# Performance work log

Hardware: AMD Instinct MI355X
Metric: run time of the kernel (lower is better)

The kernel has to match this reference:

```python
import jax, jax.numpy as jnp
import numpy as np

N_NODES = 50000


def gcn_conv(x, edge_index, W, b, n_nodes):
    # Linear transform first (as in PyG GCNConv), then normalized aggregation
    xw = x @ W  # [N, out]
    src, dst = edge_index[0], edge_index[1]
    loops = jnp.arange(n_nodes, dtype=src.dtype)
    s = jnp.concatenate([src, loops])  # add self-loops
    d = jnp.concatenate([dst, loops])
    deg = jax.ops.segment_sum(jnp.ones_like(s, dtype=xw.dtype), d, num_segments=n_nodes)
    dinv = jnp.where(deg > 0, jax.lax.rsqrt(deg), 0.0)
    norm = dinv[s] * dinv[d]  # [E+N]
    msg = xw[s] * norm[:, None]  # gather + scale
    out = jax.ops.segment_sum(msg, d, num_segments=n_nodes)  # scatter-add
    return out + b


def setup_inputs() -> dict:
    key = jax.random.key(0)
    k1, k2, k3, k4 = jax.random.split(key, 4)
    in_dim, hidden = 128, 128
    n_edges = 625000
    x = jax.random.normal(k1, (N_NODES, in_dim), dtype=jnp.float32)
    edge_index = jax.random.randint(k2, (2, n_edges), 0, N_NODES, dtype=jnp.int64)
    # glorot-ish scale
    W1 = jax.random.normal(k3, (in_dim, hidden), dtype=jnp.float32) * (1.0 / np.sqrt(in_dim))
    b1 = jnp.zeros((hidden,), dtype=jnp.float32)
    W2 = jax.random.normal(k4, (hidden, hidden), dtype=jnp.float32) * (1.0 / np.sqrt(hidden))
    b2 = jnp.zeros((hidden,), dtype=jnp.float32)
    return {"x": x, "edge_index": edge_index, "W1": W1, "b1": b1, "W2": W2, "b2": b2}


def reference(x, edge_index, W1, b1, W2, b2):
    n = x.shape[0]
    h = gcn_conv(x, edge_index, W1, b1, n)
    h = jax.nn.relu(h)
    # dropout(p=0.3) is identity in eval mode
    h = gcn_conv(h, edge_index, W2, b2, n)
    return jax.nn.relu(h)
```

## Files before the change

### kernel.cpp

```cpp
#include <hip/hip_runtime.h>
#include <hip/hip_bf16.h>

#define NNODES 50000
#define BKT 64
#define LP 136
#define NC 25
#define CCAP 40960
#define P0EPT 16
#define FINE 256
#define AGG_BLOCKS 2048

typedef short bf16x8 __attribute__((ext_vector_type(8)));
typedef float f32x4 __attribute__((ext_vector_type(4)));

__device__ __forceinline__ unsigned short f2bf_rn(float f) {
    unsigned int u = __float_as_uint(f);
    return (unsigned short)((u + 0x7fffu + ((u >> 16) & 1u)) >> 16);
}
__device__ __forceinline__ float bf_lo(unsigned int u) { return __uint_as_float(u << 16); }
__device__ __forceinline__ float bf_hi(unsigned int u) { return __uint_as_float(u & 0xffff0000u); }


__global__ __launch_bounds__(256) void k_prep(const float* __restrict__ W1,
                                              const float* __restrict__ W2,
                                              unsigned short* __restrict__ WT1,
                                              unsigned short* __restrict__ WT2,
                                              const int* __restrict__ src,
                                              const int* __restrict__ dst,
                                              int* __restrict__ gcnt,
                                              unsigned int* __restrict__ rec, int E) {
    __shared__ float tile[128 * 129];
    int b = blockIdx.x, t = threadIdx.x;
    if (b < 2) {
        const float* W = b ? W2 : W1;
        unsigned short* WT = b ? WT2 : WT1;
        for (int idx = t; idx < 128 * 128; idx += 256)
            tile[(idx >> 7) * 129 + (idx & 127)] = W[idx];
        __syncthreads();
        for (int idx = t; idx < 128 * 128; idx += 256) {
            int c = idx >> 7, k = idx & 127;
            WT[c * 128 + k] = f2bf_rn(tile[k * 129 + c]);
        }
        return;
    }
    int* lhist = (int*)tile;
    int* lbase = lhist + NC;
    if (t < NC) lhist[t] = 0;
    __syncthreads();

    int e0 = ((b - 2) * 256 + t) * P0EPT;
    unsigned int r[P0EPT];
    int cc[P0EPT];
    int lofs[P0EPT];
    int nv = 0;
    if (e0 + P0EPT <= E) {
#pragma unroll
        for (int k4 = 0; k4 < P0EPT / 4; ++k4) {
            int4 s4 = *(const int4*)&src[e0 + k4 * 4];
            int4 d4 = *(const int4*)&dst[e0 + k4 * 4];
            int ss[4] = {s4.x, s4.y, s4.z, s4.w};
            int dd[4] = {d4.x, d4.y, d4.z, d4.w};
#pragma unroll
            for (int k = 0; k < 4; ++k) {
                r[k4 * 4 + k] = (unsigned)(ss[k] & 0xffff) | ((unsigned)dd[k] << 16);
                cc[k4 * 4 + k] = dd[k] >> 11;
            }
        }
        nv = P0EPT;
    } else {
#pragma unroll
        for (int k = 0; k < P0EPT; ++k) {
            int e = e0 + k;
            if (e < E) {
                int s = src[e], d = dst[e];
                r[k] = (unsigned)(s & 0xffff) | ((unsigned)d << 16);
                cc[k] = d >> 11;
                nv = k + 1;
            } else {
                cc[k] = 0;
            }
        }
    }
#pragma unroll
    for (int k = 0; k < P0EPT; ++k)
        if (k < nv) lofs[k] = atomicAdd(&lhist[cc[k]], 1);
    __syncthreads();
    if (t < NC) lbase[t] = atomicAdd(&gcnt[t], lhist[t]);
    __syncthreads();
#pragma unroll
    for (int k = 0; k < P0EPT; ++k)
        if (k < nv) {
            int pos = lbase[cc[k]] + lofs[k];
            if (pos < CCAP) rec[(size_t)cc[k] * CCAP + pos] = r[k];
        }
}


__global__ __launch_bounds__(256) void k_build(const unsigned int* __restrict__ rec,
                                               const int* __restrict__ gcnt,
                                               int* __restrict__ cnt,
                                               unsigned short* __restrict__ bkt,
                                               float* __restrict__ dinv,
                                               const float* __restrict__ X,
                                               const unsigned short* __restrict__ WT,
                                               unsigned short* __restrict__ Yb,
                                               int n, int P1B) {
    __shared__ __align__(16) unsigned char smem[FINE * BKT * 2 + FINE * 4];
    int t = threadIdx.x, b = blockIdx.x;
    if (b < P1B) {
        unsigned short* lbkt = (unsigned short*)smem;
        int* lcnt = (int*)(smem + FINE * BKT * 2);
        int lo = b * FINE;
        int c = lo >> 11;
        for (int i = t; i < FINE; i += 256) lcnt[i] = 0;
        __syncthreads();

        int M = min(gcnt[c], CCAP);
        const unsigned int* R = &rec[(size_t)c * CCAP];
        auto process = [&](unsigned int rv) {
            unsigned dl = (rv >> 16) - (unsigned)lo;
            if (dl < (unsigned)FINE) {
                int p = atomicAdd(&lcnt[dl], 1);
                if (p < BKT) lbkt[dl * BKT + p] = (unsigned short)(rv & 0xffffu);
            }
        };
        int M4 = M >> 2;
        for (int i = t; i < M4; i += 256) {
            uint4 q = *(const uint4*)&R[i * 4];
            process(q.x); process(q.y); process(q.z); process(q.w);
        }
        for (int i = (M4 << 2) + t; i < M; i += 256) process(R[i]);
        __syncthreads();

        if (lo + t < n) {
            int cv = lcnt[t];
            cnt[lo + t] = cv;
            dinv[lo + t] = rsqrtf((float)cv + 1.0f);
        }
        for (int i = t; i < FINE * 8; i += 256) {
            int node = i >> 3;
            if (lo + node < n)
                ((uint4*)&bkt[(size_t)lo * BKT])[i] = ((const uint4*)lbkt)[i];
        }
        return;
    }
    unsigned short* Ep = (unsigned short*)smem;
    int gb = b - P1B;
    int lane = t & 63, w = t >> 6;
    int m = lane & 15, quad = lane >> 4;
    int base = gb * 64 + w * 16;
    int row = min(base + m, n - 1);

    bf16x8 a[4];
#pragma unroll
    for (int kt = 0; kt < 4; ++kt) {
        const float* pa = &X[(size_t)row * 128 + kt * 32 + quad * 8];
        float4 v0 = *(const float4*)pa;
        float4 v1 = *(const float4*)(pa + 4);
        a[kt][0] = (short)f2bf_rn(v0.x); a[kt][1] = (short)f2bf_rn(v0.y);
        a[kt][2] = (short)f2bf_rn(v0.z); a[kt][3] = (short)f2bf_rn(v0.w);
        a[kt][4] = (short)f2bf_rn(v1.x); a[kt][5] = (short)f2bf_rn(v1.y);
        a[kt][6] = (short)f2bf_rn(v1.z); a[kt][7] = (short)f2bf_rn(v1.w);
    }

    f32x4 acc[8];
#pragma unroll
    for (int i = 0; i < 8; ++i) acc[i] = f32x4{0.f, 0.f, 0.f, 0.f};
#pragma unroll
    for (int kt = 0; kt < 4; ++kt) {
        int ko = kt * 32 + quad * 8;
#pragma unroll
        for (int ct = 0; ct < 8; ++ct) {
            bf16x8 bfrag = *(const bf16x8*)&WT[(ct * 16 + m) * 128 + ko];
            acc[ct] = __builtin_amdgcn_mfma_f32_16x16x32_bf16(a[kt], bfrag, acc[ct], 0, 0, 0);
        }
    }

    unsigned short* ep = &Ep[w * 16 * LP];
#pragma unroll
    for (int ct = 0; ct < 8; ++ct)
#pragma unroll
        for (int r = 0; r < 4; ++r)
            ep[(quad * 4 + r) * LP + ct * 16 + m] = f2bf_rn(acc[ct][r]);
    __syncthreads();
    int rr = lane & 15, cc2 = lane >> 4;
    int orow = base + rr;
    if (orow < n) {
#pragma unroll
        for (int i2 = 0; i2 < 4; ++i2)
            ((uint4*)&Yb[(size_t)orow * 128])[cc2 * 4 + i2] =
                *(const uint4*)&ep[rr * LP + (cc2 * 4 + i2) * 8];
    }
}


__device__ __forceinline__ void gather_wsum(const unsigned int* __restrict__ xwb,
                                            const float* __restrict__ dinv,
                                            const unsigned short* __restrict__ bp,
                                            int degc, int lane,
                                            float& ax, float& ay) {
    float px = 0.f, py = 0.f;
    int j = 0;
    for (; j + 8 <= degc; j += 8) {
        int4 q = *(const int4*)&bp[j];
        int s0 = q.x & 0xffff, s1 = (int)((unsigned)q.x >> 16);
        int s2 = q.y & 0xffff, s3 = (int)((unsigned)q.y >> 16);
        int s4 = q.z & 0xffff, s5 = (int)((unsigned)q.z >> 16);
        int s6 = q.w & 0xffff, s7 = (int)((unsigned)q.w >> 16);
        unsigned int u0 = xwb[(size_t)s0 * 64 + lane];
        unsigned int u1 = xwb[(size_t)s1 * 64 + lane];
        unsigned int u2 = xwb[(size_t)s2 * 64 + lane];
        unsigned int u3 = xwb[(size_t)s3 * 64 + lane];
        unsigned int u4 = xwb[(size_t)s4 * 64 + lane];
        unsigned int u5 = xwb[(size_t)s5 * 64 + lane];
        unsigned int u6 = xwb[(size_t)s6 * 64 + lane];
        unsigned int u7 = xwb[(size_t)s7 * 64 + lane];
        float w0 = dinv[s0], w1 = dinv[s1], w2 = dinv[s2], w3 = dinv[s3];
        float w4 = dinv[s4], w5 = dinv[s5], w6 = dinv[s6], w7 = dinv[s7];
        ax = fmaf(bf_lo(u0), w0, ax);  ay = fmaf(bf_hi(u0), w0, ay);
        px = fmaf(bf_lo(u1), w1, px);  py = fmaf(bf_hi(u1), w1, py);
        ax = fmaf(bf_lo(u2), w2, ax);  ay = fmaf(bf_hi(u2), w2, ay);
        px = fmaf(bf_lo(u3), w3, px);  py = fmaf(bf_hi(u3), w3, py);
        ax = fmaf(bf_lo(u4), w4, ax);  ay = fmaf(bf_hi(u4), w4, ay);
        px = fmaf(bf_lo(u5), w5, px);  py = fmaf(bf_hi(u5), w5, py);
        ax = fmaf(bf_lo(u6), w6, ax);  ay = fmaf(bf_hi(u6), w6, ay);
        px = fmaf(bf_lo(u7), w7, px);  py = fmaf(bf_hi(u7), w7, py);
    }
    if (j + 4 <= degc) {
        int2 q = *(const int2*)&bp[j];
        int s0 = q.x & 0xffff, s1 = (int)((unsigned)q.x >> 16);
        int s2 = q.y & 0xffff, s3 = (int)((unsigned)q.y >> 16);
        unsigned int u0 = xwb[(size_t)s0 * 64 + lane];
        unsigned int u1 = xwb[(size_t)s1 * 64 + lane];
        unsigned int u2 = xwb[(size_t)s2 * 64 + lane];
        unsigned int u3 = xwb[(size_t)s3 * 64 + lane];
        float w0 = dinv[s0], w1 = dinv[s1], w2 = dinv[s2], w3 = dinv[s3];
        ax = fmaf(bf_lo(u0), w0, ax);  ay = fmaf(bf_hi(u0), w0, ay);
        px = fmaf(bf_lo(u1), w1, px);  py = fmaf(bf_hi(u1), w1, py);
        ax = fmaf(bf_lo(u2), w2, ax);  ay = fmaf(bf_hi(u2), w2, ay);
        px = fmaf(bf_lo(u3), w3, px);  py = fmaf(bf_hi(u3), w3, py);
        j += 4;
    }
    for (; j < degc; ++j) {
        int s = bp[j];
        float wv = dinv[s];
        unsigned int u = xwb[(size_t)s * 64 + lane];
        ax = fmaf(bf_lo(u), wv, ax);
        ay = fmaf(bf_hi(u), wv, ay);
    }
    ax += px;
    ay += py;
}


__device__ __forceinline__ void gather_sum(const unsigned int* __restrict__ xwb,
                                           const unsigned short* __restrict__ bp,
                                           int degc, int lane,
                                           float& ax, float& ay) {
    float px = 0.f, py = 0.f;
    int j = 0;
    for (; j + 8 <= degc; j += 8) {
        int4 q = *(const int4*)&bp[j];
        int s0 = q.x & 0xffff, s1 = (int)((unsigned)q.x >> 16);
        int s2 = q.y & 0xffff, s3 = (int)((unsigned)q.y >> 16);
        int s4 = q.z & 0xffff, s5 = (int)((unsigned)q.z >> 16);
        int s6 = q.w & 0xffff, s7 = (int)((unsigned)q.w >> 16);
        unsigned int u0 = xwb[(size_t)s0 * 64 + lane];
        unsigned int u1 = xwb[(size_t)s1 * 64 + lane];
        unsigned int u2 = xwb[(size_t)s2 * 64 + lane];
        unsigned int u3 = xwb[(size_t)s3 * 64 + lane];
        unsigned int u4 = xwb[(size_t)s4 * 64 + lane];
        unsigned int u5 = xwb[(size_t)s5 * 64 + lane];
        unsigned int u6 = xwb[(size_t)s6 * 64 + lane];
        unsigned int u7 = xwb[(size_t)s7 * 64 + lane];
        ax += bf_lo(u0);  ay += bf_hi(u0);
        px += bf_lo(u1);  py += bf_hi(u1);
        ax += bf_lo(u2);  ay += bf_hi(u2);
        px += bf_lo(u3);  py += bf_hi(u3);
        ax += bf_lo(u4);  ay += bf_hi(u4);
        px += bf_lo(u5);  py += bf_hi(u5);
        ax += bf_lo(u6);  ay += bf_hi(u6);
        px += bf_lo(u7);  py += bf_hi(u7);
    }
    if (j + 4 <= degc) {
        int2 q = *(const int2*)&bp[j];
        int s0 = q.x & 0xffff, s1 = (int)((unsigned)q.x >> 16);
        int s2 = q.y & 0xffff, s3 = (int)((unsigned)q.y >> 16);
        unsigned int u0 = xwb[(size_t)s0 * 64 + lane];
        unsigned int u1 = xwb[(size_t)s1 * 64 + lane];
        unsigned int u2 = xwb[(size_t)s2 * 64 + lane];
        unsigned int u3 = xwb[(size_t)s3 * 64 + lane];
        ax += bf_lo(u0);  ay += bf_hi(u0);
        px += bf_lo(u1);  py += bf_hi(u1);
        ax += bf_lo(u2);  ay += bf_hi(u2);
        px += bf_lo(u3);  py += bf_hi(u3);
        j += 4;
    }
    for (; j < degc; ++j) {
        int s = bp[j];
        unsigned int u = xwb[(size_t)s * 64 + lane];
        ax += bf_lo(u);
        ay += bf_hi(u);
    }
    ax += px;
    ay += py;
}


__global__ __launch_bounds__(1024, 8) void k_aggemm(const unsigned int* __restrict__ xw1,
                                                    const int* __restrict__ cnt,
                                                    const unsigned short* __restrict__ bkt,
                                                    const float* __restrict__ dinv,
                                                    const float* __restrict__ bias,
                                                    const unsigned short* __restrict__ WT2,
                                                    unsigned short* __restrict__ xw2, int n) {
    __shared__ unsigned short Wl[128 * LP];
    __shared__ unsigned short At[64 * LP];
    __shared__ float dsw[64];
    int t = threadIdx.x, lane = t & 63, w = t >> 6;
    int m = lane & 15, quad = lane >> 4;
    int base = blockIdx.x * 64;

    for (int idx = t; idx < 128 * 16; idx += 1024) {
        int r = idx >> 4, c8 = (idx & 15) << 3;
        *(uint4*)&Wl[r * LP + c8] = *(const uint4*)&WT2[r * 128 + c8];
    }
    float bx = bias[lane * 2], by = bias[lane * 2 + 1];

#pragma unroll
    for (int k = 0; k < 4; ++k) {
        int nd = w * 4 + k;
        int i = min(base + nd, n - 1);
        int degc = min(cnt[i], BKT);
        float di = dinv[i];
        unsigned int v0 = xw1[(size_t)i * 64 + lane];
        float ax = di * bf_lo(v0), ay = di * bf_hi(v0);
        gather_wsum(xw1, dinv, &bkt[(size_t)i * BKT], degc, lane, ax, ay);
        ax = fmaxf(fmaf(di, ax, bx), 0.0f);
        ay = fmaxf(fmaf(di, ay, by), 0.0f);
        ((unsigned int*)&At[nd * LP])[lane] =
            (unsigned)f2bf_rn(ax) | ((unsigned)f2bf_rn(ay) << 16);
        if (lane == 0) dsw[nd] = di;
    }
    __syncthreads();

    int ct = w & 7, rb = w >> 3;
    f32x4 acc0 = f32x4{0.f, 0.f, 0.f, 0.f};
    f32x4 acc1 = f32x4{0.f, 0.f, 0.f, 0.f};
#pragma unroll
    for (int kt = 0; kt < 4; ++kt) {
        int ko = kt * 32 + quad * 8;
        bf16x8 bfrag = *(const bf16x8*)&Wl[(ct * 16 + m) * LP + ko];
        bf16x8 a0 = *(const bf16x8*)&At[(rb * 16 + m) * LP + ko];
        bf16x8 a1 = *(const bf16x8*)&At[((rb + 2) * 16 + m) * LP + ko];
        acc0 = __builtin_amdgcn_mfma_f32_16x16x32_bf16(a0, bfrag, acc0, 0, 0, 0);
        acc1 = __builtin_amdgcn_mfma_f32_16x16x32_bf16(a1, bfrag, acc1, 0, 0, 0);
    }
    __syncthreads();

#pragma unroll
    for (int r = 0; r < 4; ++r) {
        int r0 = rb * 16 + quad * 4 + r;
        int r1 = (rb + 2) * 16 + quad * 4 + r;
        At[r0 * LP + ct * 16 + m] = f2bf_rn(acc0[r] * dsw[r0]);
        At[r1 * LP + ct * 16 + m] = f2bf_rn(acc1[r] * dsw[r1]);
    }
    __syncthreads();

    int row = t >> 4, q = t & 15;
    int orow = base + row;
    if (orow < n)
        *(uint4*)&xw2[(size_t)orow * 128 + q * 8] = *(const uint4*)&At[row * LP + q * 8];
}


__global__ __launch_bounds__(256) void k_agg(const unsigned int* __restrict__ xwb,
                                             const int* __restrict__ cnt,
                                             const unsigned short* __restrict__ bkt,
                                             const float* __restrict__ dinv,
                                             const float* __restrict__ bias,
                                             float* __restrict__ out, int n) {
    int lane = threadIdx.x & 63;
    int gw = (blockIdx.x * 256 + threadIdx.x) >> 6;
    int nw = (gridDim.x * 256) >> 6;
    float bx = bias[lane * 2], by = bias[lane * 2 + 1];
    for (int i = gw; i < n; i += nw) {
        int degc = min(cnt[i], BKT);
        float di = dinv[i];
        unsigned int v0 = xwb[(size_t)i * 64 + lane];
        float ax = bf_lo(v0), ay = bf_hi(v0);
        gather_sum(xwb, &bkt[(size_t)i * BKT], degc, lane, ax, ay);
        ax = fmaxf(fmaf(di, ax, bx), 0.0f);
        ay = fmaxf(fmaf(di, ay, by), 0.0f);
        ((float2*)out)[(size_t)i * 64 + lane] = make_float2(ax, ay);
    }
}


extern "C" void kernel_launch(void* const* d_in, const int* in_sizes, int n_in,
                              void* d_out, int out_size, void* d_ws, size_t ws_size,
                              hipStream_t stream) {
    const float* x  = (const float*)d_in[0];
    const int*   ei = (const int*)d_in[1];
    const float* W1 = (const float*)d_in[2];
    const float* b1 = (const float*)d_in[3];
    const float* W2 = (const float*)d_in[4];
    const float* b2 = (const float*)d_in[5];
    float* out = (float*)d_out;

    const int N = NNODES;
    const int E = in_sizes[1] / 2;
    const int* src = ei;
    const int* dst = ei + E;

    char* p = (char*)d_ws;
    size_t off = 0;
    auto take = [&](size_t bytes) -> void* {
        void* r = p + off;
        off = (off + bytes + 255) & ~(size_t)255;
        return r;
    };
    int* cnt = (int*)take((size_t)N * 4);
    unsigned short* bkt = (unsigned short*)take((size_t)N * BKT * 2);
    unsigned short* w1t = (unsigned short*)take(128 * 128 * 2);
    unsigned short* w2t = (unsigned short*)take(128 * 128 * 2);
    unsigned short* xw1 = (unsigned short*)take((size_t)N * 128 * 2);
    unsigned short* xw2 = (unsigned short*)take((size_t)N * 128 * 2);
    float* dinv = (float*)take((size_t)N * 4);
    int* gcnt = (int*)take(NC * 4);
    unsigned int* rec = (unsigned int*)take((size_t)NC * CCAP * 4);

    const int P0B = (E + 256 * P0EPT - 1) / (256 * P0EPT);
    const int P1B = (N + FINE - 1) / FINE;
    const int GB = (N + 63) / 64;

    hipMemsetAsync(gcnt, 0, NC * sizeof(int), stream);
    k_prep<<<2 + P0B, 256, 0, stream>>>(W1, W2, w1t, w2t, src, dst, gcnt, rec, E);
    k_build<<<P1B + GB, 256, 0, stream>>>(rec, gcnt, cnt, bkt, dinv, x, w1t, xw1, N, P1B);
    k_aggemm<<<GB, 1024, 0, stream>>>((const unsigned int*)xw1, cnt, bkt, dinv,
                                      b1, w2t, xw2, N);
    k_agg<<<AGG_BLOCKS, 256, 0, stream>>>((const unsigned int*)xw2, cnt, bkt, dinv,
                                          b2, out, N);
}
```

Measured before the change: 179.7 us.

## Use finer coarse buckets and sentinel-padded bucket lists for half-wave gather

```diff
diff --git a/kernel.cpp b/kernel.cpp
--- a/kernel.cpp
+++ b/kernel.cpp
@@ -4,10 +4,11 @@
 #define NNODES 50000
 #define BKT 64
 #define LP 136
-#define NC 25
-#define CCAP 40960
+#define NC 196
+#define CCAP 4096
 #define P0EPT 16
 #define FINE 256
+#define SENT 50000
 #define AGG_BLOCKS 2048
 
 typedef short bf16x8 __attribute__((ext_vector_type(8)));
@@ -28,10 +29,20 @@
                                               const int* __restrict__ src,
                                               const int* __restrict__ dst,
                                               int* __restrict__ gcnt,
-                                              unsigned int* __restrict__ rec, int E) {
+                                              unsigned int* __restrict__ rec,
+                                              unsigned short* __restrict__ xw1,
+                                              unsigned short* __restrict__ xw2,
+                                              float* __restrict__ dinv, int E) {
     __shared__ float tile[128 * 129];
     int b = blockIdx.x, t = threadIdx.x;
     if (b < 2) {
+        if (b == 0) {
+            if (t < 64) {
+                ((unsigned int*)&xw1[(size_t)NNODES * 128])[t] = 0;
+                ((unsigned int*)&xw2[(size_t)NNODES * 128])[t] = 0;
+            }
+            if (t == 64) dinv[NNODES] = 0.0f;
+        }
         const float* W = b ? W2 : W1;
         unsigned short* WT = b ? WT2 : WT1;
         for (int idx = t; idx < 128 * 128; idx += 256)
@@ -63,7 +74,7 @@
 #pragma unroll
             for (int k = 0; k < 4; ++k) {
                 r[k4 * 4 + k] = (unsigned)(ss[k] & 0xffff) | ((unsigned)dd[k] << 16);
-                cc[k4 * 4 + k] = dd[k] >> 11;
+                cc[k4 * 4 + k] = dd[k] >> 8;
             }
         }
         nv = P0EPT;
@@ -74,7 +85,7 @@
             if (e < E) {
                 int s = src[e], d = dst[e];
                 r[k] = (unsigned)(s & 0xffff) | ((unsigned)d << 16);
-                cc[k] = d >> 11;
+                cc[k] = d >> 8;
                 nv = k + 1;
             } else {
                 cc[k] = 0;
@@ -111,12 +122,13 @@
         unsigned short* lbkt = (unsigned short*)smem;
         int* lcnt = (int*)(smem + FINE * BKT * 2);
         int lo = b * FINE;
-        int c = lo >> 11;
-        for (int i = t; i < FINE; i += 256) lcnt[i] = 0;
+        const unsigned int sent2 = (unsigned)SENT | ((unsigned)SENT << 16);
+        for (int i = t; i < FINE * BKT / 2; i += 256) ((unsigned int*)lbkt)[i] = sent2;
+        if (t < FINE) lcnt[t] = 0;
         __syncthreads();
 
-        int M = min(gcnt[c], CCAP);
-        const unsigned int* R = &rec[(size_t)c * CCAP];
+        int M = min(gcnt[b], CCAP);
+        const unsigned int* R = &rec[(size_t)b * CCAP];
         auto process = [&](unsigned int rv) {
             unsigned dl = (rv >> 16) - (unsigned)lo;
             if (dl < (unsigned)FINE) {
@@ -253,57 +265,35 @@
 }
 
 
-__device__ __forceinline__ void gather_sum(const unsigned int* __restrict__ xwb,
-                                           const unsigned short* __restrict__ bp,
-                                           int degc, int lane,
-                                           float& ax, float& ay) {
-    float px = 0.f, py = 0.f;
-    int j = 0;
-    for (; j + 8 <= degc; j += 8) {
-        int4 q = *(const int4*)&bp[j];
+__device__ __forceinline__ void gather_sum16(const unsigned int* __restrict__ xwb,
+                                             const unsigned short* __restrict__ bp,
+                                             int degc, int sub, int half,
+                                             float& a0, float& a1, float& a2, float& a3) {
+    float p0 = 0.f, p1 = 0.f, p2 = 0.f, p3 = 0.f;
+    for (int j = 0; j < degc; j += 16) {
+        int4 q = *(const int4*)&bp[j + half * 8];
         int s0 = q.x & 0xffff, s1 = (int)((unsigned)q.x >> 16);
         int s2 = q.y & 0xffff, s3 = (int)((unsigned)q.y >> 16);
         int s4 = q.z & 0xffff, s5 = (int)((unsigned)q.z >> 16);
         int s6 = q.w & 0xffff, s7 = (int)((unsigned)q.w >> 16);
-        unsigned int u0 = xwb[(size_t)s0 * 64 + lane];
-        unsigned int u1 = xwb[(size_t)s1 * 64 + lane];
-        unsigned int u2 = xwb[(size_t)s2 * 64 + lane];
-        unsigned int u3 = xwb[(size_t)s3 * 64 + lane];
-        unsigned int u4 = xwb[(size_t)s4 * 64 + lane];
-        unsigned int u5 = xwb[(size_t)s5 * 64 + lane];
-        unsigned int u6 = xwb[(size_t)s6 * 64 + lane];
-        unsigned int u7 = xwb[(size_t)s7 * 64 + lane];
-        ax += bf_lo(u0);  ay += bf_hi(u0);
-        px += bf_lo(u1);  py += bf_hi(u1);
-        ax += bf_lo(u2);  ay += bf_hi(u2);
-        px += bf_lo(u3);  py += bf_hi(u3);
-        ax += bf_lo(u4);  ay += bf_hi(u4);
-        px += bf_lo(u5);  py += bf_hi(u5);
-        ax += bf_lo(u6);  ay += bf_hi(u6);
-        px += bf_lo(u7);  py += bf_hi(u7);
-    }
-    if (j + 4 <= degc) {
-        int2 q = *(const int2*)&bp[j];
-        int s0 = q.x & 0xffff, s1 = (int)((unsigned)q.x >> 16);
-        int s2 = q.y & 0xffff, s3 = (int)((unsigned)q.y >> 16);
-        unsigned int u0 = xwb[(size_t)s0 * 64 + lane];
-        unsigned int u1 = xwb[(size_t)s1 * 64 + lane];
-        unsigned int u2 = xwb[(size_t)s2 * 64 + lane];
-        unsigned int u3 = xwb[(size_t)s3 * 64 + lane];
-        ax += bf_lo(u0);  ay += bf_hi(u0);
-        px += bf_lo(u1);  py += bf_hi(u1);
-        ax += bf_lo(u2);  ay += bf_hi(u2);
-        px += bf_lo(u3);  py += bf_hi(u3);
-        j += 4;
-    }
-    for (; j < degc; ++j) {
-        int s = bp[j];
-        unsigned int u = xwb[(size_t)s * 64 + lane];
-        ax += bf_lo(u);
-        ay += bf_hi(u);
-    }
-    ax += px;
-    ay += py;
+        uint2 u0 = *(const uint2*)&xwb[(size_t)s0 * 64 + sub * 2];
+        uint2 u1 = *(const uint2*)&xwb[(size_t)s1 * 64 + sub * 2];
+        uint2 u2 = *(const uint2*)&xwb[(size_t)s2 * 64 + sub * 2];
+        uint2 u3 = *(const uint2*)&xwb[(size_t)s3 * 64 + sub * 2];
+        uint2 u4 = *(const uint2*)&xwb[(size_t)s4 * 64 + sub * 2];
+        uint2 u5 = *(const uint2*)&xwb[(size_t)s5 * 64 + sub * 2];
+        uint2 u6 = *(const uint2*)&xwb[(size_t)s6 * 64 + sub * 2];
+        uint2 u7 = *(const uint2*)&xwb[(size_t)s7 * 64 + sub * 2];
+        a0 += bf_lo(u0.x); a1 += bf_hi(u0.x); a2 += bf_lo(u0.y); a3 += bf_hi(u0.y);
+        p0 += bf_lo(u1.x); p1 += bf_hi(u1.x); p2 += bf_lo(u1.y); p3 += bf_hi(u1.y);
+        a0 += bf_lo(u2.x); a1 += bf_hi(u2.x); a2 += bf_lo(u2.y); a3 += bf_hi(u2.y);
+        p0 += bf_lo(u3.x); p1 += bf_hi(u3.x); p2 += bf_lo(u3.y); p3 += bf_hi(u3.y);
+        a0 += bf_lo(u4.x); a1 += bf_hi(u4.x); a2 += bf_lo(u4.y); a3 += bf_hi(u4.y);
+        p0 += bf_lo(u5.x); p1 += bf_hi(u5.x); p2 += bf_lo(u5.y); p3 += bf_hi(u5.y);
+        a0 += bf_lo(u6.x); a1 += bf_hi(u6.x); a2 += bf_lo(u6.y); a3 += bf_hi(u6.y);
+        p0 += bf_lo(u7.x); p1 += bf_hi(u7.x); p2 += bf_lo(u7.y); p3 += bf_hi(u7.y);
+    }
+    a0 += p0; a1 += p1; a2 += p2; a3 += p3;
 }
 
 
@@ -381,18 +371,30 @@
                                              const float* __restrict__ bias,
                                              float* __restrict__ out, int n) {
     int lane = threadIdx.x & 63;
+    int sub = lane & 31, half = lane >> 5;
     int gw = (blockIdx.x * 256 + threadIdx.x) >> 6;
     int nw = (gridDim.x * 256) >> 6;
-    float bx = bias[lane * 2], by = bias[lane * 2 + 1];
+    float4 bv = *(const float4*)&bias[sub * 4];
     for (int i = gw; i < n; i += nw) {
         int degc = min(cnt[i], BKT);
         float di = dinv[i];
-        unsigned int v0 = xwb[(size_t)i * 64 + lane];
-        float ax = bf_lo(v0), ay = bf_hi(v0);
-        gather_sum(xwb, &bkt[(size_t)i * BKT], degc, lane, ax, ay);
-        ax = fmaxf(fmaf(di, ax, bx), 0.0f);
-        ay = fmaxf(fmaf(di, ay, by), 0.0f);
-        ((float2*)out)[(size_t)i * 64 + lane] = make_float2(ax, ay);
+        float a0 = 0.f, a1 = 0.f, a2 = 0.f, a3 = 0.f;
+        if (half) {
+            uint2 v = *(const uint2*)&xwb[(size_t)i * 64 + sub * 2];
+            a0 = bf_lo(v.x); a1 = bf_hi(v.x); a2 = bf_lo(v.y); a3 = bf_hi(v.y);
+        }
+        gather_sum16(xwb, &bkt[(size_t)i * BKT], degc, sub, half, a0, a1, a2, a3);
+        a0 += __shfl(a0, lane ^ 32);
+        a1 += __shfl(a1, lane ^ 32);
+        a2 += __shfl(a2, lane ^ 32);
+        a3 += __shfl(a3, lane ^ 32);
+        if (!half) {
+            a0 = fmaxf(fmaf(di, a0, bv.x), 0.0f);
+            a1 = fmaxf(fmaf(di, a1, bv.y), 0.0f);
+            a2 = fmaxf(fmaf(di, a2, bv.z), 0.0f);
+            a3 = fmaxf(fmaf(di, a3, bv.w), 0.0f);
+            *(float4*)&out[(size_t)i * 128 + sub * 4] = make_float4(a0, a1, a2, a3);
+        }
     }
 }
 
@@ -424,9 +426,9 @@
     unsigned short* bkt = (unsigned short*)take((size_t)N * BKT * 2);
     unsigned short* w1t = (unsigned short*)take(128 * 128 * 2);
     unsigned short* w2t = (unsigned short*)take(128 * 128 * 2);
-    unsigned short* xw1 = (unsigned short*)take((size_t)N * 128 * 2);
-    unsigned short* xw2 = (unsigned short*)take((size_t)N * 128 * 2);
-    float* dinv = (float*)take((size_t)N * 4);
+    unsigned short* xw1 = (unsigned short*)take((size_t)(N + 1) * 128 * 2);
+    unsigned short* xw2 = (unsigned short*)take((size_t)(N + 1) * 128 * 2);
+    float* dinv = (float*)take((size_t)(N + 1) * 4);
     int* gcnt = (int*)take(NC * 4);
     unsigned int* rec = (unsigned int*)take((size_t)NC * CCAP * 4);
 
@@ -435,7 +437,8 @@
     const int GB = (N + 63) / 64;
 
     hipMemsetAsync(gcnt, 0, NC * sizeof(int), stream);
-    k_prep<<<2 + P0B, 256, 0, stream>>>(W1, W2, w1t, w2t, src, dst, gcnt, rec, E);
+    k_prep<<<2 + P0B, 256, 0, stream>>>(W1, W2, w1t, w2t, src, dst, gcnt, rec,
+                                        xw1, xw2, dinv, E);
     k_build<<<P1B + GB, 256, 0, stream>>>(rec, gcnt, cnt, bkt, dinv, x, w1t, xw1, N, P1B);
     k_aggemm<<<GB, 1024, 0, stream>>>((const unsigned int*)xw1, cnt, bkt, dinv,
                                       b1, w2t, xw2, N);
```

New measurement: 177.1 us (median of 2 runs). About the same (-1.4%).
